# Kernel optimization log

Hardware: AMD Instinct MI355X
Metric: run time of the kernel (lower is better)

The kernel has to match this reference:

```python
import jax, jax.numpy as jnp
import numpy as np

B, N, F, W = 32, 512, 6, 128
K_GRAPH, K_POINT, HOPS = 100, 3, 2
CONV_D, POINT_D, LIN_D = 3, 3, 5
DIM2 = 2 * CONV_D * W + 2 * POINT_D * W  # 1536


def setup_inputs() -> dict:
    key = jax.random.key(0)
    ks = jax.random.split(key, 12)
    g = lambda i, shape, s=0.05: jax.random.normal(ks[i], shape, jnp.float32) * s
    return {
        'x': jax.random.normal(ks[0], (B * N, F), jnp.float32),
        'batch': jnp.repeat(jnp.arange(B, dtype=jnp.int32), N),  # equal-size graphs
        'tag1_W': g(1, (HOPS + 1, F, W)),
        'tag1_b': jnp.zeros((W,), jnp.float32),
        'tag_W': g(2, (CONV_D - 1, HOPS + 1, W, W)),
        'tag_b': jnp.zeros((CONV_D - 1, W), jnp.float32),
        'p1_W1': g(3, (2 * F, W)), 'p1_b1': jnp.zeros((W,), jnp.float32),
        'p1_W2': g(4, (W, W)), 'p1_b2': jnp.zeros((W,), jnp.float32),
        'pf_W': g(5, (POINT_D - 1, 2 * W, W)), 'pf_b': jnp.zeros((POINT_D - 1, W), jnp.float32),
        'bn_gamma': jnp.ones((DIM2,), jnp.float32), 'bn_beta': jnp.zeros((DIM2,), jnp.float32),
        'lin_W': g(6, (LIN_D, DIM2, DIM2), 0.02), 'lin_b': jnp.zeros((LIN_D, DIM2), jnp.float32),
        'out_W': g(7, (DIM2, 1)), 'out_b': jnp.zeros((1,), jnp.float32),
    }


def _knn(xb, k):
    # xb: [B,N,C] -> per-graph kNN source indices [B,N,k] (self excluded)
    sq = jnp.sum(xb * xb, axis=-1)
    d = sq[:, :, None] + sq[:, None, :] - 2.0 * jnp.einsum('bnc,bmc->bnm', xb, xb)
    d = d + jnp.eye(xb.shape[1], dtype=xb.dtype) * 1e10  # exclude self loops
    _, idx = jax.lax.top_k(-d, k)
    return idx


def _gather(xb, idx):
    # xb [B,N,C], idx [B,N,k] -> neighbor features [B,N,k,C]
    return jax.vmap(lambda xv, iv: xv[iv])(xb, idx)


def _tag(xb, nbr, Wk, b):
    # TAGConv K=2: every node has in-degree K_GRAPH, so sym gcn_norm edge weight
    # = deg^-1/2[src]*deg^-1/2[dst] = 1/k  ->  one hop == neighbor mean.
    out = jnp.einsum('bnc,cd->bnd', xb, Wk[0])
    h = xb
    for k in range(1, Wk.shape[0]):
        h = jnp.mean(_gather(h, nbr), axis=2)
        out = out + jnp.einsum('bnc,cd->bnd', h, Wk[k])
    return out + b


def _edgeconv(yb, k, mlp):
    # DynamicEdgeConv: rebuild kNN on current features, msg = mlp([x_i, x_j - x_i]), max-aggr
    nbr = _knn(yb, k)
    yj = _gather(yb, nbr)                       # [B,N,k,C]
    yi = jnp.broadcast_to(yb[:, :, None, :], yj.shape)
    m = mlp(jnp.concatenate([yi, yj - yi], axis=-1))
    return jnp.max(m, axis=2)


def reference(x, batch, tag1_W, tag1_b, tag_W, tag_b, p1_W1, p1_b1, p1_W2, p1_b2,
              pf_W, pf_b, bn_gamma, bn_beta, lin_W, lin_b, out_W, out_b):
    lrelu = jax.nn.leaky_relu  # negative_slope=0.01 matches torch default
    xb = x.reshape(B, N, -1)   # batch = repeat(arange(B), N), equal-size graphs
    nbr = _knn(xb, K_GRAPH)    # dropout_adj / Dropout: eval mode (identity)

    h = lrelu(_tag(xb, nbr, tag1_W, tag1_b))
    pools = [jnp.concatenate([h.mean(axis=1), h.max(axis=1)], axis=-1)]  # gap||gmp
    for f in range(CONV_D - 1):
        h = lrelu(_tag(h, nbr, tag_W[f], tag_b[f]))
        pools.append(jnp.concatenate([h.mean(axis=1), h.max(axis=1)], axis=-1))
    xc = jnp.concatenate(pools, axis=-1)  # [B, 2*CONV_D*W]

    mlp1 = lambda z: lrelu(lrelu(z @ p1_W1 + p1_b1) @ p1_W2 + p1_b2)
    y = _edgeconv(xb, K_POINT, mlp1)
    ylist = [y]
    for f in range(POINT_D - 1):
        y = _edgeconv(y, K_POINT, lambda z, f=f: lrelu(z @ pf_W[f] + pf_b[f]))
        ylist.append(y)
    y = jnp.concatenate(ylist, axis=-1)  # [B,N,POINT_D*W]
    yc = jnp.concatenate([y.mean(axis=1), y.max(axis=1)], axis=-1)

    z = jnp.concatenate([xc, yc], axis=-1)  # [B, DIM2]
    mu = z.mean(axis=0)
    var = jnp.mean((z - mu) ** 2, axis=0)
    z = (z - mu) / jnp.sqrt(var + 1e-5) * bn_gamma + bn_beta  # BatchNorm1d (batch stats)
    for g in range(LIN_D):
        z = lrelu(z @ lin_W[g] + lin_b[g])
    z = z @ out_W + out_b  # classification=False -> no sigmoid
    return z.reshape(-1)
```

## Files before the change

kernel.cpp:

```cpp
#include <hip/hip_runtime.h>
#include <hip/hip_bf16.h>

#define Bg 32
#define Nn 512
#define Fdim 6
#define Wd 128
#define KG 100
#define KP 3
#define DIM2 1536
#define GC16 16
#define NSL 12
#define KSL 128

typedef __hip_bfloat16 bf16;
typedef unsigned long long ull;

__device__ __forceinline__ float b2f(bf16 v) { return __bfloat162float(v); }
__device__ __forceinline__ float h2f(unsigned short h) { return __uint_as_float((unsigned)h << 16); }
__device__ __forceinline__ float lrelu(float v) { return v > 0.0f ? v : 0.01f * v; }

__global__ void detect_kernel(const unsigned short* __restrict__ x, int* __restrict__ flag) {
  if (threadIdx.x == 0 && blockIdx.x == 0) {
    int big = 0;
    for (int i = 0; i < 512; i += 2) {
      unsigned short u = x[i];
      int e = (u >> 7) & 0xFF;
      if (e >= 140) big++;
    }
    *flag = (big > 20) ? 1 : 0;
  }
}

__global__ void convert_kernel(const void* __restrict__ x, float* __restrict__ xf, int n,
                               const int* __restrict__ flag) {
  int i = blockIdx.x * 256 + threadIdx.x;
  if (i >= n) return;
  if (*flag) xf[i] = ((const float*)x)[i];
  else       xf[i] = b2f(((const bf16*)x)[i]);
}

__device__ __forceinline__ void ins3b(ull key, ull& k0, ull& k1, ull& k2) {
  ull M0 = k0 < key ? key : k0;  k0 = k0 < key ? k0 : key;
  ull M1 = k1 < M0 ? M0 : k1;    k1 = k1 < M0 ? k1 : M0;
  k2 = k2 < M1 ? k2 : M1;
}

__global__ void knn100_kernel(const float* __restrict__ xf, int* __restrict__ nbr) {
  __shared__ float xg[Nn * 7];
  __shared__ float sqv[Nn];
  int t = threadIdx.x; int w = t >> 6; int l = t & 63;
  int row0 = blockIdx.x * 4; int g = row0 >> 9;
  const float* xp = xf + g * (Nn * Fdim);
  for (int j = t; j < Nn; j += 256) {
    float s = 0.0f;
    #pragma unroll
    for (int c = 0; c < Fdim; c++) { float v = xp[j * Fdim + c]; xg[j * 7 + c] = v; s += v * v; }
    sqv[j] = s;
  }
  __syncthreads();
  int i = (row0 & 511) + w;
  float xi[Fdim];
  #pragma unroll
  for (int c = 0; c < Fdim; c++) xi[c] = xg[i * 7 + c];
  float sqi = sqv[i];
  unsigned m[8];
  #pragma unroll
  for (int ch = 0; ch < 8; ch++) {
    int j = ch * 64 + l;
    float dot = 0.0f;
    #pragma unroll
    for (int c = 0; c < Fdim; c++) dot += xi[c] * xg[j * 7 + c];
    float d = sqi + sqv[j] - 2.0f * dot;
    if (j == i) d += 1e10f;
    unsigned u = __float_as_uint(d);
    m[ch] = (u & 0x80000000u) ? ~u : (u | 0x80000000u);
  }
  unsigned T = 0u;
  for (int b = 31; b >= 0; b--) {
    unsigned mid = T | (1u << b);
    int c = 0;
    #pragma unroll
    for (int ch = 0; ch < 8; ch++) c += __popcll(__ballot(m[ch] < mid));
    if (c < KG) T = mid;
  }
  int* outp = nbr + ((size_t)(g * Nn + i)) * KG;
  ull lmask = (1ull << l) - 1ull;
  int base = 0;
  #pragma unroll
  for (int ch = 0; ch < 8; ch++) {
    bool less = m[ch] < T;
    ull bal = __ballot(less);
    if (less) outp[base + __popcll(bal & lmask)] = ch * 64 + l;
    base += __popcll(bal);
  }
  int need = KG - base;
  int eqb = 0;
  #pragma unroll
  for (int ch = 0; ch < 8; ch++) {
    bool eq = (m[ch] == T);
    ull bal = __ballot(eq);
    int gr = eqb + __popcll(bal & lmask);
    if (eq && gr < need) outp[base + gr] = ch * 64 + l;
    eqb += __popcll(bal);
  }
}

__global__ void knn3_x_kernel(const float* __restrict__ xf, int* __restrict__ nbr) {
  __shared__ float xg[Nn * 7];
  __shared__ float sqv[Nn];
  int t = threadIdx.x; int bid = blockIdx.x;
  int g = bid >> 5;
  const float* xp = xf + g * (Nn * Fdim);
  for (int j = t; j < Nn; j += 256) {
    float s = 0.0f;
    #pragma unroll
    for (int c = 0; c < Fdim; c++) { float v = xp[j * Fdim + c]; xg[j * 7 + c] = v; s += v * v; }
    sqv[j] = s;
  }
  __syncthreads();
  int lr = t >> 4; int sub = t & 15; int l = t & 63;
  int i = ((bid & 31) << 4) + lr;
  float xi[Fdim];
  #pragma unroll
  for (int c = 0; c < Fdim; c++) xi[c] = xg[i * 7 + c];
  float sqi = sqv[i];
  ull k0 = ~0ull, k1 = ~0ull, k2 = ~0ull;
  for (int jj = 0; jj < 32; jj++) {
    int s = (jj + l) & 31;
    int j = sub * 32 + s;
    float dot = 0.0f;
    #pragma unroll
    for (int c = 0; c < Fdim; c++) dot += xi[c] * xg[j * 7 + c];
    float d = sqi + sqv[j] - 2.0f * dot;
    if (j == i) d += 1e10f;
    unsigned u = __float_as_uint(d);
    unsigned m = (u & 0x80000000u) ? ~u : (u | 0x80000000u);
    ins3b(((ull)m << 32) | (unsigned)j, k0, k1, k2);
  }
  #pragma unroll
  for (int off = 1; off <= 8; off <<= 1) {
    ull b0 = __shfl_xor(k0, off, 64);
    ull b1 = __shfl_xor(k1, off, 64);
    ull b2 = __shfl_xor(k2, off, 64);
    ins3b(b0, k0, k1, k2); ins3b(b1, k0, k1, k2); ins3b(b2, k0, k1, k2);
  }
  if (sub == 0) {
    int row = g * Nn + i;
    nbr[row * 3 + 0] = (int)(k0 & 0xFFFFFFFFu);
    nbr[row * 3 + 1] = (int)(k1 & 0xFFFFFFFFu);
    nbr[row * 3 + 2] = (int)(k2 & 0xFFFFFFFFu);
  }
}

__global__ void knn3_gram_kernel(const float* __restrict__ G, int* __restrict__ nbr, int g0) {
  __shared__ float sqv[Nn];
  int t = threadIdx.x; int bid = blockIdx.x;
  int gl = bid >> 5; int g = g0 + gl;
  const float* Gg = G + (size_t)gl * Nn * Nn;
  for (int j = t; j < Nn; j += 256) sqv[j] = Gg[(size_t)j * Nn + j];
  __syncthreads();
  int lr = t >> 4; int sub = t & 15; int l = t & 63;
  int i = ((bid & 31) << 4) + lr;
  float sqi = sqv[i];
  const float* Gr = Gg + (size_t)i * Nn;
  ull k0 = ~0ull, k1 = ~0ull, k2 = ~0ull;
  for (int jj = 0; jj < 32; jj++) {
    int s = (jj + l) & 31;
    int j = sub * 32 + s;
    float d = sqi + sqv[j] - 2.0f * Gr[j];
    if (j == i) d += 1e10f;
    unsigned u = __float_as_uint(d);
    unsigned m = (u & 0x80000000u) ? ~u : (u | 0x80000000u);
    ins3b(((ull)m << 32) | (unsigned)j, k0, k1, k2);
  }
  #pragma unroll
  for (int off = 1; off <= 8; off <<= 1) {
    ull b0 = __shfl_xor(k0, off, 64);
    ull b1 = __shfl_xor(k1, off, 64);
    ull b2 = __shfl_xor(k2, off, 64);
    ins3b(b0, k0, k1, k2); ins3b(b1, k0, k1, k2); ins3b(b2, k0, k1, k2);
  }
  if (sub == 0) {
    int row = g * Nn + i;
    nbr[row * 3 + 0] = (int)(k0 & 0xFFFFFFFFu);
    nbr[row * 3 + 1] = (int)(k1 & 0xFFFFFFFFu);
    nbr[row * 3 + 2] = (int)(k2 & 0xFFFFFFFFu);
  }
}

__global__ void gm6_kernel(const float* __restrict__ src, const int* __restrict__ nbr,
                           float* __restrict__ dst) {
  __shared__ float s[Nn * Fdim];
  int g = blockIdx.x; int t = threadIdx.x;
  const float* sp = src + g * (Nn * Fdim);
  for (int idx = t; idx < Nn * Fdim; idx += 512) s[idx] = sp[idx];
  __syncthreads();
  float acc[Fdim] = {0, 0, 0, 0, 0, 0};
  const int* nb = nbr + ((size_t)(g * Nn + t)) * KG;
  for (int k = 0; k < KG; k++) {
    int j = nb[k];
    #pragma unroll
    for (int c = 0; c < Fdim; c++) acc[c] += s[j * Fdim + c];
  }
  float* dp = dst + (size_t)(g * Nn + t) * Fdim;
  #pragma unroll
  for (int c = 0; c < Fdim; c++) dp[c] = acc[c] / 100.0f;
}

__global__ void gm128_kernel(const float* __restrict__ src, const int* __restrict__ nbr,
                             float* __restrict__ dst) {
  __shared__ int ids[8][KG];
  int t = threadIdx.x;
  int row0 = blockIdx.x * 8; int g = row0 >> 9;
  for (int idx = t; idx < 8 * KG; idx += 256) {
    int r = idx / KG, k = idx - r * KG;
    ids[r][k] = nbr[(size_t)(row0 + r) * KG + k];
  }
  __syncthreads();
  int lane = t & 31, r = t >> 5;
  const float4* sp = (const float4*)(src + (size_t)g * Nn * Wd);
  float ax = 0.0f, ay = 0.0f, az = 0.0f, aw = 0.0f;
  #pragma unroll 5
  for (int k = 0; k < KG; k++) {
    float4 v = sp[ids[r][k] * 32 + lane];
    ax += v.x; ay += v.y; az += v.z; aw += v.w;
  }
  float4 o = make_float4(ax / 100.0f, ay / 100.0f, az / 100.0f, aw / 100.0f);
  ((float4*)(dst + (size_t)(row0 + r) * Wd))[lane] = o;
}

__global__ void proj3_kernel(const float* __restrict__ in0, const float* __restrict__ in1,
                             const float* __restrict__ in2, const void* __restrict__ Wt_,
                             const void* __restrict__ bt_, float* __restrict__ out,
                             const int* __restrict__ flag) {
  __shared__ float s0[48], s1[48], s2[48];
  int t = threadIdx.x;
  int node0 = blockIdx.x * 8;
  int f32 = *flag;
  float acc[8] = {0, 0, 0, 0, 0, 0, 0, 0};
  float bd;
  if (t < 48) {
    s0[t] = in0[(size_t)node0 * 6 + t];
    s1[t] = in1[(size_t)node0 * 6 + t];
    s2[t] = in2[(size_t)node0 * 6 + t];
  }
  __syncthreads();
  if (f32) {
    const float* W = (const float*)Wt_;
    for (int c = 0; c < 6; c++) {
      float w0 = W[c * 128 + t], w1 = W[(6 + c) * 128 + t], w2 = W[(12 + c) * 128 + t];
      #pragma unroll
      for (int n = 0; n < 8; n++)
        acc[n] += s0[n * 6 + c] * w0 + s1[n * 6 + c] * w1 + s2[n * 6 + c] * w2;
    }
    bd = ((const float*)bt_)[t];
  } else {
    const bf16* W = (const bf16*)Wt_;
    for (int c = 0; c < 6; c++) {
      float w0 = b2f(W[c * 128 + t]), w1 = b2f(W[(6 + c) * 128 + t]), w2 = b2f(W[(12 + c) * 128 + t]);
      #pragma unroll
      for (int n = 0; n < 8; n++)
        acc[n] += s0[n * 6 + c] * w0 + s1[n * 6 + c] * w1 + s2[n * 6 + c] * w2;
    }
    bd = b2f(((const bf16*)bt_)[t]);
  }
  #pragma unroll
  for (int n = 0; n < 8; n++)
    out[(size_t)(node0 + n) * 128 + t] = lrelu(acc[n] + bd);
}

__global__ void proj3_big_kernel(const float* __restrict__ in0, const float* __restrict__ in1,
                                 const float* __restrict__ in2, const void* __restrict__ Wt_,
                                 const void* __restrict__ bt_, float* __restrict__ out,
                                 long Woff, long boff, const int* __restrict__ flag) {
  __shared__ __align__(16) float sa[3][32 * 128];
  __shared__ __align__(16) float Wc[64 * 128];
  int t = threadIdx.x;
  int node0 = blockIdx.x * 32;
  int f32 = *flag;
  {
    const float4* q0 = (const float4*)(in0 + (size_t)node0 * 128);
    const float4* q1 = (const float4*)(in1 + (size_t)node0 * 128);
    const float4* q2 = (const float4*)(in2 + (size_t)node0 * 128);
    float4* s0 = (float4*)sa[0]; float4* s1 = (float4*)sa[1]; float4* s2 = (float4*)sa[2];
    #pragma unroll
    for (int it = 0; it < 4; it++) {
      s0[t + it * 256] = q0[t + it * 256];
      s1[t + it * 256] = q1[t + it * 256];
      s2[t + it * 256] = q2[t + it * 256];
    }
  }
  int tx = t & 31, ty = t >> 5;
  int col0 = tx * 4, n0 = ty * 4;
  float acc[4][4];
  #pragma unroll
  for (int n = 0; n < 4; n++)
    #pragma unroll
    for (int j = 0; j < 4; j++) acc[n][j] = 0.0f;
  for (int half = 0; half < 6; half++) {
    int a = half >> 1, h = half & 1;
    {
      float4* Wl = (float4*)Wc;
      if (f32) {
        const float4* Wg = (const float4*)((const float*)Wt_ + Woff
                                           + (size_t)a * 16384 + (size_t)h * 8192);
        #pragma unroll
        for (int i = 0; i < 8; i++) Wl[t + i * 256] = Wg[t + i * 256];
      } else {
        const ushort4* Wg = (const ushort4*)((const unsigned short*)Wt_ + Woff
                                             + (size_t)a * 16384 + (size_t)h * 8192);
        #pragma unroll
        for (int i = 0; i < 8; i++) {
          ushort4 hh = Wg[t + i * 256];
          Wl[t + i * 256] = make_float4(h2f(hh.x), h2f(hh.y), h2f(hh.z), h2f(hh.w));
        }
      }
    }
    __syncthreads();
    const float* sp = sa[a];
    int cbase = h * 64;
    #pragma unroll 4
    for (int cc0 = 0; cc0 < 64; cc0 += 4) {
      float wv[4][4];
      #pragma unroll
      for (int cc = 0; cc < 4; cc++) {
        float4 w4 = *(const float4*)&Wc[(cc0 + cc) * 128 + col0];
        wv[cc][0] = w4.x; wv[cc][1] = w4.y; wv[cc][2] = w4.z; wv[cc][3] = w4.w;
      }
      int c0 = cbase + cc0;
      #pragma unroll
      for (int n = 0; n < 4; n++) {
        float4 av = *(const float4*)&sp[(n0 + n) * 128 + c0];
        #pragma unroll
        for (int j = 0; j < 4; j++)
          acc[n][j] += av.x * wv[0][j] + av.y * wv[1][j] + av.z * wv[2][j] + av.w * wv[3][j];
      }
    }
    __syncthreads();
  }
  float bdv[4];
  if (f32) {
    const float* bt = (const float*)bt_ + boff;
    #pragma unroll
    for (int j = 0; j < 4; j++) bdv[j] = bt[col0 + j];
  } else {
    const bf16* bt = (const bf16*)bt_ + boff;
    #pragma unroll
    for (int j = 0; j < 4; j++) bdv[j] = b2f(bt[col0 + j]);
  }
  #pragma unroll
  for (int n = 0; n < 4; n++) {
    float4 ov;
    ov.x = lrelu(acc[n][0] + bdv[0]); ov.y = lrelu(acc[n][1] + bdv[1]);
    ov.z = lrelu(acc[n][2] + bdv[2]); ov.w = lrelu(acc[n][3] + bdv[3]);
    *(float4*)&out[(size_t)(node0 + n0 + n) * 128 + col0] = ov;
  }
}

__global__ void proj_dual_kernel(const float* __restrict__ in, const void* __restrict__ Wt_,
                                 float* __restrict__ u, float* __restrict__ v,
                                 const int* __restrict__ flag) {
  __shared__ float s0[48];
  int t = threadIdx.x; int node0 = blockIdx.x * 8;
  int f32 = *flag;
  float au[8] = {0, 0, 0, 0, 0, 0, 0, 0};
  float av[8] = {0, 0, 0, 0, 0, 0, 0, 0};
  if (t < 48) s0[t] = in[(size_t)node0 * 6 + t];
  __syncthreads();
  if (f32) {
    const float* W = (const float*)Wt_;
    for (int c = 0; c < 6; c++) {
      float wa = W[c * 128 + t], wb = W[(6 + c) * 128 + t];
      #pragma unroll
      for (int n = 0; n < 8; n++) { float x = s0[n * 6 + c]; au[n] += x * wa; av[n] += x * wb; }
    }
  } else {
    const bf16* W = (const bf16*)Wt_;
    for (int c = 0; c < 6; c++) {
      float wa = b2f(W[c * 128 + t]), wb = b2f(W[(6 + c) * 128 + t]);
      #pragma unroll
      for (int n = 0; n < 8; n++) { float x = s0[n * 6 + c]; au[n] += x * wa; av[n] += x * wb; }
    }
  }
  #pragma unroll
  for (int n = 0; n < 8; n++) {
    u[(size_t)(node0 + n) * 128 + t] = au[n];
    v[(size_t)(node0 + n) * 128 + t] = av[n];
  }
}

__global__ void proj_dual_big_kernel(const float* __restrict__ in, const void* __restrict__ Wt_,
                                     float* __restrict__ u, float* __restrict__ v,
                                     long Woff, const int* __restrict__ flag) {
  __shared__ __align__(16) float sa[32 * 128];
  __shared__ __align__(16) float Wc[64 * 128];
  int t = threadIdx.x;
  int node0 = blockIdx.x * 32;
  int f32 = *flag;
  {
    const float4* qp = (const float4*)(in + (size_t)node0 * 128);
    float4* s0 = (float4*)sa;
    #pragma unroll
    for (int it = 0; it < 4; it++) s0[t + it * 256] = qp[t + it * 256];
  }
  int tx = t & 31, ty = t >> 5;
  int col0 = tx * 4, n0 = ty * 4;
  float accu[4][4], accv[4][4];
  #pragma unroll
  for (int n = 0; n < 4; n++)
    #pragma unroll
    for (int j = 0; j < 4; j++) { accu[n][j] = 0.0f; accv[n][j] = 0.0f; }
  for (int q = 0; q < 4; q++) {
    {
      float4* Wl = (float4*)Wc;
      if (f32) {
        const float4* Wg = (const float4*)((const float*)Wt_ + Woff + (size_t)q * 8192);
        #pragma unroll
        for (int i = 0; i < 8; i++) Wl[t + i * 256] = Wg[t + i * 256];
      } else {
        const ushort4* Wg = (const ushort4*)((const unsigned short*)Wt_ + Woff
                                             + (size_t)q * 8192);
        #pragma unroll
        for (int i = 0; i < 8; i++) {
          ushort4 hh = Wg[t + i * 256];
          Wl[t + i * 256] = make_float4(h2f(hh.x), h2f(hh.y), h2f(hh.z), h2f(hh.w));
        }
      }
    }
    __syncthreads();
    int cbase = (q & 1) * 64;
    if (q < 2) {
      #pragma unroll 4
      for (int cc0 = 0; cc0 < 64; cc0 += 4) {
        float wv[4][4];
        #pragma unroll
        for (int cc = 0; cc < 4; cc++) {
          float4 w4 = *(const float4*)&Wc[(cc0 + cc) * 128 + col0];
          wv[cc][0] = w4.x; wv[cc][1] = w4.y; wv[cc][2] = w4.z; wv[cc][3] = w4.w;
        }
        int c0 = cbase + cc0;
        #pragma unroll
        for (int n = 0; n < 4; n++) {
          float4 av = *(const float4*)&sa[(n0 + n) * 128 + c0];
          #pragma unroll
          for (int j = 0; j < 4; j++)
            accu[n][j] += av.x * wv[0][j] + av.y * wv[1][j] + av.z * wv[2][j] + av.w * wv[3][j];
        }
      }
    } else {
      #pragma unroll 4
      for (int cc0 = 0; cc0 < 64; cc0 += 4) {
        float wv[4][4];
        #pragma unroll
        for (int cc = 0; cc < 4; cc++) {
          float4 w4 = *(const float4*)&Wc[(cc0 + cc) * 128 + col0];
          wv[cc][0] = w4.x; wv[cc][1] = w4.y; wv[cc][2] = w4.z; wv[cc][3] = w4.w;
        }
        int c0 = cbase + cc0;
        #pragma unroll
        for (int n = 0; n < 4; n++) {
          float4 av = *(const float4*)&sa[(n0 + n) * 128 + c0];
          #pragma unroll
          for (int j = 0; j < 4; j++)
            accv[n][j] += av.x * wv[0][j] + av.y * wv[1][j] + av.z * wv[2][j] + av.w * wv[3][j];
        }
      }
    }
    __syncthreads();
  }
  #pragma unroll
  for (int n = 0; n < 4; n++) {
    *(float4*)&u[(size_t)(node0 + n0 + n) * 128 + col0] = *(float4*)accu[n];
    *(float4*)&v[(size_t)(node0 + n0 + n) * 128 + col0] = *(float4*)accv[n];
  }
}

__global__ void edge_mlp1_kernel(const float* __restrict__ u, const float* __restrict__ v,
                                 const int* __restrict__ nbrp, const void* __restrict__ W2_,
                                 const void* __restrict__ b1_, const void* __restrict__ b2_,
                                 float* __restrict__ y, const int* __restrict__ flag) {
  __shared__ __align__(16) float Ws[64 * 128];
  __shared__ __align__(16) float tl[24][128];
  int t = threadIdx.x;
  int node0 = blockIdx.x * 8; int g = node0 >> 9;
  int f32 = *flag;
  if (f32) {
    const float4* Wg = (const float4*)W2_;
    float4* Wl = (float4*)Ws;
    #pragma unroll
    for (int i = 0; i < 8; i++) Wl[t + i * 256] = Wg[t + i * 256];
  } else {
    const ushort4* Wg = (const ushort4*)W2_;
    float4* Wl = (float4*)Ws;
    #pragma unroll
    for (int i = 0; i < 8; i++) {
      ushort4 h = Wg[t + i * 256];
      Wl[t + i * 256] = make_float4(h2f(h.x), h2f(h.y), h2f(h.z), h2f(h.w));
    }
  }
  {
    int lane = t & 31, n = t >> 5;
    int row = node0 + n;
    float4 ui = ((const float4*)(u + (size_t)row * 128))[lane];
    float4 vi = ((const float4*)(v + (size_t)row * 128))[lane];
    float4 b1v;
    if (f32) b1v = ((const float4*)b1_)[lane];
    else {
      ushort4 h = ((const ushort4*)b1_)[lane];
      b1v = make_float4(h2f(h.x), h2f(h.y), h2f(h.z), h2f(h.w));
    }
    float4 base = make_float4(ui.x - vi.x + b1v.x, ui.y - vi.y + b1v.y,
                              ui.z - vi.z + b1v.z, ui.w - vi.w + b1v.w);
    #pragma unroll
    for (int k = 0; k < 3; k++) {
      int j = nbrp[row * 3 + k];
      float4 vj = ((const float4*)(v + (size_t)(g * Nn + j) * 128))[lane];
      float4 tv;
      tv.x = lrelu(base.x + vj.x); tv.y = lrelu(base.y + vj.y);
      tv.z = lrelu(base.z + vj.z); tv.w = lrelu(base.w + vj.w);
      *(float4*)&tl[n * 3 + k][lane * 4] = tv;
    }
  }
  __syncthreads();
  int tx = t & 31, ty = t >> 5;
  int col0 = tx * 4;
  float acc[3][4];
  #pragma unroll
  for (int k = 0; k < 3; k++)
    #pragma unroll
    for (int j = 0; j < 4; j++) acc[k][j] = 0.0f;
  #pragma unroll 4
  for (int cc0 = 0; cc0 < 64; cc0 += 4) {
    float wv[4][4];
    #pragma unroll
    for (int cc = 0; cc < 4; cc++) {
      float4 w4 = *(const float4*)&Ws[(cc0 + cc) * 128 + col0];
      wv[cc][0] = w4.x; wv[cc][1] = w4.y; wv[cc][2] = w4.z; wv[cc][3] = w4.w;
    }
    #pragma unroll
    for (int k = 0; k < 3; k++) {
      float4 av = *(const float4*)&tl[ty * 3 + k][cc0];
      #pragma unroll
      for (int j = 0; j < 4; j++)
        acc[k][j] += av.x * wv[0][j] + av.y * wv[1][j] + av.z * wv[2][j] + av.w * wv[3][j];
    }
  }
  __syncthreads();
  if (f32) {
    const float4* Wg = (const float4*)W2_ + 2048;
    float4* Wl = (float4*)Ws;
    #pragma unroll
    for (int i = 0; i < 8; i++) Wl[t + i * 256] = Wg[t + i * 256];
  } else {
    const ushort4* Wg = (const ushort4*)W2_ + 2048;
    float4* Wl = (float4*)Ws;
    #pragma unroll
    for (int i = 0; i < 8; i++) {
      ushort4 h = Wg[t + i * 256];
      Wl[t + i * 256] = make_float4(h2f(h.x), h2f(h.y), h2f(h.z), h2f(h.w));
    }
  }
  __syncthreads();
  #pragma unroll 4
  for (int cc0 = 0; cc0 < 64; cc0 += 4) {
    float wv[4][4];
    #pragma unroll
    for (int cc = 0; cc < 4; cc++) {
      float4 w4 = *(const float4*)&Ws[(cc0 + cc) * 128 + col0];
      wv[cc][0] = w4.x; wv[cc][1] = w4.y; wv[cc][2] = w4.z; wv[cc][3] = w4.w;
    }
    #pragma unroll
    for (int k = 0; k < 3; k++) {
      float4 av = *(const float4*)&tl[ty * 3 + k][64 + cc0];
      #pragma unroll
      for (int j = 0; j < 4; j++)
        acc[k][j] += av.x * wv[0][j] + av.y * wv[1][j] + av.z * wv[2][j] + av.w * wv[3][j];
    }
  }
  float b2d[4];
  if (f32) {
    const float* b2p = (const float*)b2_;
    #pragma unroll
    for (int j = 0; j < 4; j++) b2d[j] = b2p[col0 + j];
  } else {
    const bf16* b2p = (const bf16*)b2_;
    #pragma unroll
    for (int j = 0; j < 4; j++) b2d[j] = b2f(b2p[col0 + j]);
  }
  float4 ov;
  {
    float m0 = lrelu(acc[0][0] + b2d[0]);
    m0 = fmaxf(m0, lrelu(acc[1][0] + b2d[0]));
    ov.x = fmaxf(m0, lrelu(acc[2][0] + b2d[0]));
    float m1 = lrelu(acc[0][1] + b2d[1]);
    m1 = fmaxf(m1, lrelu(acc[1][1] + b2d[1]));
    ov.y = fmaxf(m1, lrelu(acc[2][1] + b2d[1]));
    float m2 = lrelu(acc[0][2] + b2d[2]);
    m2 = fmaxf(m2, lrelu(acc[1][2] + b2d[2]));
    ov.z = fmaxf(m2, lrelu(acc[2][2] + b2d[2]));
    float m3 = lrelu(acc[0][3] + b2d[3]);
    m3 = fmaxf(m3, lrelu(acc[1][3] + b2d[3]));
    ov.w = fmaxf(m3, lrelu(acc[2][3] + b2d[3]));
  }
  *(float4*)&y[(size_t)(node0 + ty) * 128 + col0] = ov;
}

__global__ void edge_max_kernel(const float* __restrict__ u, const float* __restrict__ v,
                                const int* __restrict__ nbrp, const void* __restrict__ bias_,
                                float* __restrict__ y, long boff, const int* __restrict__ flag) {
  int row = blockIdx.x; int g = row >> 9; int t = threadIdx.x;
  float ui = u[(size_t)row * 128 + t], vi = v[(size_t)row * 128 + t];
  float bd;
  if (*flag) bd = ((const float*)bias_ + boff)[t]; else bd = b2f(((const bf16*)bias_ + boff)[t]);
  float m = -3.4e38f;
  #pragma unroll
  for (int k = 0; k < 3; k++) {
    int j = nbrp[row * 3 + k];
    m = fmaxf(m, lrelu(ui - vi + v[(size_t)(g * Nn + j) * 128 + t] + bd));
  }
  y[(size_t)row * 128 + t] = m;
}

__global__ void gram_kernel(const float* __restrict__ y, float* __restrict__ G, int g0) {
  __shared__ float As[64][17], Bs[64][17];
  int bid = blockIdx.x;
  int gl = bid >> 6; int tt = bid & 63; int ti = tt >> 3; int tj = tt & 7;
  int g = g0 + gl;
  int t = threadIdx.x; int tx = t & 15, ty = t >> 4;
  const float* Yg = y + (size_t)g * Nn * Wd;
  float* Gg = G + (size_t)gl * Nn * Nn;
  float c[4][4];
  #pragma unroll
  for (int p = 0; p < 4; p++)
    #pragma unroll
    for (int q = 0; q < 4; q++) c[p][q] = 0.0f;
  for (int k0 = 0; k0 < 128; k0 += 16) {
    for (int idx = t; idx < 1024; idx += 256) {
      int r = idx >> 4, cc = idx & 15;
      As[r][cc] = Yg[(ti * 64 + r) * 128 + k0 + cc];
      Bs[r][cc] = Yg[(tj * 64 + r) * 128 + k0 + cc];
    }
    __syncthreads();
    for (int kk = 0; kk < 16; kk++) {
      float a[4], bb[4];
      #pragma unroll
      for (int p = 0; p < 4; p++) a[p] = As[ty * 4 + p][kk];
      #pragma unroll
      for (int q = 0; q < 4; q++) bb[q] = Bs[tx * 4 + q][kk];
      #pragma unroll
      for (int p = 0; p < 4; p++)
        #pragma unroll
        for (int q = 0; q < 4; q++) c[p][q] += a[p] * bb[q];
    }
    __syncthreads();
  }
  #pragma unroll
  for (int p = 0; p < 4; p++)
    #pragma unroll
    for (int q = 0; q < 4; q++)
      Gg[(size_t)(ti * 64 + ty * 4 + p) * Nn + tj * 64 + tx * 4 + q] = c[p][q];
}

__global__ void pool1_kernel(const float* __restrict__ h, float* __restrict__ pp) {
  int b = blockIdx.x;
  int g = b >> 3, ch = b & 7;
  int t = threadIdx.x;
  const float* hg = h + (size_t)g * Nn * Wd + (size_t)ch * 64 * Wd;
  float s = 0.0f, m = -3.4e38f;
  #pragma unroll 4
  for (int n = 0; n < 64; n++) {
    float vv = hg[n * 128 + t];
    s += vv; m = fmaxf(m, vv);
  }
  pp[b * 256 + t] = s;
  pp[b * 256 + 128 + t] = m;
}

__global__ void pool2_kernel(const float* __restrict__ pp, float* __restrict__ z,
                             int meanoff, int maxoff) {
  int g = blockIdx.x; int t = threadIdx.x;
  float s = 0.0f, m = -3.4e38f;
  #pragma unroll
  for (int q = 0; q < 8; q++) {
    s += pp[(g * 8 + q) * 256 + t];
    m = fmaxf(m, pp[(g * 8 + q) * 256 + 128 + t]);
  }
  z[g * DIM2 + meanoff + t] = s / 512.0f;
  z[g * DIM2 + maxoff + t] = m;
}

__global__ void bn_kernel(float* __restrict__ z, const void* __restrict__ gamma,
                          const void* __restrict__ beta, const int* __restrict__ flag) {
  int c = blockIdx.x * 256 + threadIdx.x;
  if (c >= DIM2) return;
  float s = 0.0f;
  for (int r = 0; r < Bg; r++) s += z[r * DIM2 + c];
  float mu = s / 32.0f;
  float v = 0.0f;
  for (int r = 0; r < Bg; r++) { float d = z[r * DIM2 + c] - mu; v += d * d; }
  float var = v / 32.0f;
  float gm, bt;
  if (*flag) { gm = ((const float*)gamma)[c]; bt = ((const float*)beta)[c]; }
  else       { gm = b2f(((const bf16*)gamma)[c]); bt = b2f(((const bf16*)beta)[c]); }
  float scale = gm / sqrtf(var + 1e-5f);
  for (int r = 0; r < Bg; r++) z[r * DIM2 + c] = (z[r * DIM2 + c] - mu) * scale + bt;
}

__global__ void hl_part_kernel(const float* __restrict__ zin, const float* __restrict__ Pin,
                               const void* __restrict__ bin_, const void* __restrict__ W_,
                               float* __restrict__ Pout, long Woff, long binoff, int mode,
                               const int* __restrict__ flag) {
  __shared__ __align__(16) float zs[32][KSL];
  int t = threadIdx.x;
  int bd = blockIdx.x % 24, s = blockIdx.x / 24;
  int d0 = bd * 64, k0 = s * KSL;
  int f32 = *flag;
  if (mode == 0) {
    for (int idx = t; idx < 32 * KSL; idx += 256) {
      int r = idx >> 7, k = idx & 127;
      zs[r][k] = zin[r * DIM2 + k0 + k];
    }
  } else {
    for (int idx = t; idx < 32 * KSL / 4; idx += 256) {
      int r = idx >> 5, k4 = (idx & 31) * 4;
      float ax = 0.0f, ay = 0.0f, az = 0.0f, aw = 0.0f;
      const float* Pr = Pin + (size_t)r * NSL * DIM2 + k0 + k4;
      #pragma unroll
      for (int ss = 0; ss < NSL; ss++) {
        float4 p = *(const float4*)(Pr + (size_t)ss * DIM2);
        ax += p.x; ay += p.y; az += p.z; aw += p.w;
      }
      float b0, b1, b2, b3;
      if (f32) {
        const float* bp = (const float*)bin_ + binoff + k0 + k4;
        b0 = bp[0]; b1 = bp[1]; b2 = bp[2]; b3 = bp[3];
      } else {
        const bf16* bp = (const bf16*)bin_ + binoff + k0 + k4;
        b0 = b2f(bp[0]); b1 = b2f(bp[1]); b2 = b2f(bp[2]); b3 = b2f(bp[3]);
      }
      zs[r][k4 + 0] = lrelu(ax + b0);
      zs[r][k4 + 1] = lrelu(ay + b1);
      zs[r][k4 + 2] = lrelu(az + b2);
      zs[r][k4 + 3] = lrelu(aw + b3);
    }
  }
  __syncthreads();
  int lane = t & 63, rg = t >> 6;
  int d = d0 + lane, r0 = rg * 8;
  float acc[8];
  #pragma unroll
  for (int i = 0; i < 8; i++) acc[i] = 0.0f;
  if (f32) {
    const float* W = (const float*)W_ + Woff;
    for (int k = 0; k < KSL; k += 4) {
      float w0 = W[(size_t)(k0 + k) * DIM2 + d];
      float w1 = W[(size_t)(k0 + k + 1) * DIM2 + d];
      float w2 = W[(size_t)(k0 + k + 2) * DIM2 + d];
      float w3 = W[(size_t)(k0 + k + 3) * DIM2 + d];
      #pragma unroll
      for (int i = 0; i < 8; i++) {
        float4 z4 = *(const float4*)&zs[r0 + i][k];
        acc[i] += z4.x * w0 + z4.y * w1 + z4.z * w2 + z4.w * w3;
      }
    }
  } else {
    const unsigned short* W = (const unsigned short*)W_ + Woff;
    for (int k = 0; k < KSL; k += 4) {
      float w0 = h2f(W[(size_t)(k0 + k) * DIM2 + d]);
      float w1 = h2f(W[(size_t)(k0 + k + 1) * DIM2 + d]);
      float w2 = h2f(W[(size_t)(k0 + k + 2) * DIM2 + d]);
      float w3 = h2f(W[(size_t)(k0 + k + 3) * DIM2 + d]);
      #pragma unroll
      for (int i = 0; i < 8; i++) {
        float4 z4 = *(const float4*)&zs[r0 + i][k];
        acc[i] += z4.x * w0 + z4.y * w1 + z4.z * w2 + z4.w * w3;
      }
    }
  }
  float* Po = Pout + (size_t)s * DIM2 + d;
  #pragma unroll
  for (int i = 0; i < 8; i++) Po[(size_t)(r0 + i) * NSL * DIM2] = acc[i];
}

__global__ void hl_reduce_kernel(const float* __restrict__ Pin, const void* __restrict__ bin_,
                                 float* __restrict__ out, long binoff,
                                 const int* __restrict__ flag) {
  int idx = blockIdx.x * 256 + threadIdx.x;
  int r = idx / DIM2, d = idx - r * DIM2;
  float acc = 0.0f;
  const float* Pr = Pin + (size_t)r * NSL * DIM2 + d;
  #pragma unroll
  for (int s = 0; s < NSL; s++) acc += Pr[(size_t)s * DIM2];
  float b;
  if (*flag) b = ((const float*)bin_ + binoff)[d];
  else       b = b2f(((const bf16*)bin_ + binoff)[d]);
  out[r * DIM2 + d] = lrelu(acc + b);
}

__global__ void final_kernel(const float* __restrict__ zin, const void* __restrict__ outW,
                             const void* __restrict__ outb, void* __restrict__ out,
                             const int* __restrict__ flag) {
  __shared__ float red[256];
  int r = blockIdx.x, t = threadIdx.x;
  int f32 = *flag;
  float acc = 0.0f;
  if (f32) {
    const float* W = (const float*)outW;
    for (int c = t; c < DIM2; c += 256) acc += zin[r * DIM2 + c] * W[c];
  } else {
    const bf16* W = (const bf16*)outW;
    for (int c = t; c < DIM2; c += 256) acc += zin[r * DIM2 + c] * b2f(W[c]);
  }
  red[t] = acc; __syncthreads();
  for (int s = 128; s > 0; s >>= 1) { if (t < s) red[t] += red[t + s]; __syncthreads(); }
  if (t == 0) {
    float ob;
    if (f32) ob = ((const float*)outb)[0]; else ob = b2f(((const bf16*)outb)[0]);
    float val = red[0] + ob;
    if (f32) ((float*)out)[r] = val;
    else     ((bf16*)out)[r] = __float2bfloat16(val);
  }
}

extern "C" void kernel_launch(void* const* d_in, const int* in_sizes, int n_in,
                              void* d_out, int out_size, void* d_ws, size_t ws_size,
                              hipStream_t stream) {
  const void* x      = d_in[0];
  const void* tag1_W = d_in[2];
  const void* tag1_b = d_in[3];
  const void* tag_W  = d_in[4];
  const void* tag_b  = d_in[5];
  const void* p1_W1  = d_in[6];
  const void* p1_b1  = d_in[7];
  const void* p1_W2  = d_in[8];
  const void* p1_b2  = d_in[9];
  const void* pf_W   = d_in[10];
  const void* pf_b   = d_in[11];
  const void* bn_g   = d_in[12];
  const void* bn_b   = d_in[13];
  const void* lin_W  = d_in[14];
  const void* lin_b  = d_in[15];
  const void* out_W  = d_in[16];
  const void* out_b  = d_in[17];

  float* ws = (float*)d_ws;
  float* XF   = ws + 0;
  float* M16  = ws + 98304;
  float* M26  = ws + 196608;
  float* Z    = ws + 294912;
  float* ZB   = ws + 344064;
  int*   FLAG = (int*)(ws + 409600);
  int*   NBRP = (int*)(ws + 409616);
  int*   NBRG = (int*)(ws + 458768);
  float* S0   = ws + 2097168;
  float* S1   = ws + 4194320;
  float* S2   = ws + 6291472;
  float* S3   = ws + 8388624;
  float* PA   = S0;
  float* PB   = S1;
  float* PP   = M16;

  detect_kernel<<<1, 64, 0, stream>>>((const unsigned short*)x, FLAG);
  convert_kernel<<<384, 256, 0, stream>>>(x, XF, Bg * Nn * Fdim, FLAG);
  knn100_kernel<<<Bg * Nn / 4, 256, 0, stream>>>(XF, NBRG);
  knn3_x_kernel<<<Bg * Nn / 16, 256, 0, stream>>>(XF, NBRP);

  gm6_kernel<<<Bg, 512, 0, stream>>>(XF, NBRG, M16);
  gm6_kernel<<<Bg, 512, 0, stream>>>(M16, NBRG, M26);
  proj3_kernel<<<2048, 128, 0, stream>>>(XF, M16, M26, tag1_W, tag1_b, S0, FLAG);
  pool1_kernel<<<256, 128, 0, stream>>>(S0, PP);
  pool2_kernel<<<Bg, 128, 0, stream>>>(PP, Z, 0, 128);

  gm128_kernel<<<Bg * Nn / 8, 256, 0, stream>>>(S0, NBRG, S1);
  gm128_kernel<<<Bg * Nn / 8, 256, 0, stream>>>(S1, NBRG, S2);
  proj3_big_kernel<<<512, 256, 0, stream>>>(S0, S1, S2, tag_W, tag_b, S3, 0, 0, FLAG);
  pool1_kernel<<<256, 128, 0, stream>>>(S3, PP);
  pool2_kernel<<<Bg, 128, 0, stream>>>(PP, Z, 256, 384);

  gm128_kernel<<<Bg * Nn / 8, 256, 0, stream>>>(S3, NBRG, S1);
  gm128_kernel<<<Bg * Nn / 8, 256, 0, stream>>>(S1, NBRG, S2);
  proj3_big_kernel<<<512, 256, 0, stream>>>(S3, S1, S2, tag_W, tag_b, S0,
                                            3L * 128 * 128, 128, FLAG);
  pool1_kernel<<<256, 128, 0, stream>>>(S0, PP);
  pool2_kernel<<<Bg, 128, 0, stream>>>(PP, Z, 512, 640);

  proj_dual_kernel<<<2048, 128, 0, stream>>>(XF, p1_W1, S0, S1, FLAG);
  edge_mlp1_kernel<<<2048, 256, 0, stream>>>(S0, S1, NBRP, p1_W2, p1_b1, p1_b2, S2, FLAG);
  pool1_kernel<<<256, 128, 0, stream>>>(S2, PP);
  pool2_kernel<<<Bg, 128, 0, stream>>>(PP, Z, 768, 1152);

  for (int c = 0; c < Bg; c += GC16) {
    gram_kernel<<<GC16 * 64, 256, 0, stream>>>(S2, S0, c);
    knn3_gram_kernel<<<GC16 * Nn / 16, 256, 0, stream>>>(S0, NBRP, c);
  }
  proj_dual_big_kernel<<<512, 256, 0, stream>>>(S2, pf_W, S0, S1, 0, FLAG);
  edge_max_kernel<<<Bg * Nn, 128, 0, stream>>>(S0, S1, NBRP, pf_b, S3, 0, FLAG);
  pool1_kernel<<<256, 128, 0, stream>>>(S3, PP);
  pool2_kernel<<<Bg, 128, 0, stream>>>(PP, Z, 896, 1280);

  for (int c = 0; c < Bg; c += GC16) {
    gram_kernel<<<GC16 * 64, 256, 0, stream>>>(S3, S0, c);
    knn3_gram_kernel<<<GC16 * Nn / 16, 256, 0, stream>>>(S0, NBRP, c);
  }
  proj_dual_big_kernel<<<512, 256, 0, stream>>>(S3, pf_W, S0, S1, 256L * 128, FLAG);
  edge_max_kernel<<<Bg * Nn, 128, 0, stream>>>(S0, S1, NBRP, pf_b, S2, 128, FLAG);
  pool1_kernel<<<256, 128, 0, stream>>>(S2, PP);
  pool2_kernel<<<Bg, 128, 0, stream>>>(PP, Z, 1024, 1408);

  bn_kernel<<<6, 256, 0, stream>>>(Z, bn_g, bn_b, FLAG);
  hl_part_kernel<<<288, 256, 0, stream>>>(Z, nullptr, nullptr, lin_W, PA,
                                          0L * DIM2 * DIM2, 0L, 0, FLAG);
  hl_part_kernel<<<288, 256, 0, stream>>>(nullptr, PA, lin_b, lin_W, PB,
                                          1L * DIM2 * DIM2, 0L * DIM2, 1, FLAG);
  hl_part_kernel<<<288, 256, 0, stream>>>(nullptr, PB, lin_b, lin_W, PA,
                                          2L * DIM2 * DIM2, 1L * DIM2, 1, FLAG);
  hl_part_kernel<<<288, 256, 0, stream>>>(nullptr, PA, lin_b, lin_W, PB,
                                          3L * DIM2 * DIM2, 2L * DIM2, 1, FLAG);
  hl_part_kernel<<<288, 256, 0, stream>>>(nullptr, PB, lin_b, lin_W, PA,
                                          4L * DIM2 * DIM2, 3L * DIM2, 1, FLAG);
  hl_reduce_kernel<<<192, 256, 0, stream>>>(PA, lin_b, ZB, 4L * DIM2, FLAG);
  final_kernel<<<Bg, 256, 0, stream>>>(ZB, out_W, out_b, d_out, FLAG);
}
```

Baseline: 842.5 us.

## Enlarge edge_mlp1 tile to 32 nodes with 6x8 register blocking

```diff
diff --git a/kernel.cpp b/kernel.cpp
--- a/kernel.cpp
+++ b/kernel.cpp
@@ -480,9 +480,9 @@
                                  const void* __restrict__ b1_, const void* __restrict__ b2_,
                                  float* __restrict__ y, const int* __restrict__ flag) {
   __shared__ __align__(16) float Ws[64 * 128];
-  __shared__ __align__(16) float tl[24][128];
+  __shared__ __align__(16) float tl[96][128];
   int t = threadIdx.x;
-  int node0 = blockIdx.x * 8; int g = node0 >> 9;
+  int node0 = blockIdx.x * 32; int g = node0 >> 9;
   int f32 = *flag;
   if (f32) {
     const float4* Wg = (const float4*)W2_;
@@ -499,50 +499,56 @@
     }
   }
   {
-    int lane = t & 31, n = t >> 5;
-    int row = node0 + n;
-    float4 ui = ((const float4*)(u + (size_t)row * 128))[lane];
-    float4 vi = ((const float4*)(v + (size_t)row * 128))[lane];
+    int lane = t & 31, grp = t >> 5;
     float4 b1v;
     if (f32) b1v = ((const float4*)b1_)[lane];
     else {
       ushort4 h = ((const ushort4*)b1_)[lane];
       b1v = make_float4(h2f(h.x), h2f(h.y), h2f(h.z), h2f(h.w));
     }
-    float4 base = make_float4(ui.x - vi.x + b1v.x, ui.y - vi.y + b1v.y,
-                              ui.z - vi.z + b1v.z, ui.w - vi.w + b1v.w);
-    #pragma unroll
-    for (int k = 0; k < 3; k++) {
-      int j = nbrp[row * 3 + k];
-      float4 vj = ((const float4*)(v + (size_t)(g * Nn + j) * 128))[lane];
-      float4 tv;
-      tv.x = lrelu(base.x + vj.x); tv.y = lrelu(base.y + vj.y);
-      tv.z = lrelu(base.z + vj.z); tv.w = lrelu(base.w + vj.w);
-      *(float4*)&tl[n * 3 + k][lane * 4] = tv;
-    }
-  }
-  __syncthreads();
-  int tx = t & 31, ty = t >> 5;
-  int col0 = tx * 4;
-  float acc[3][4];
-  #pragma unroll
-  for (int k = 0; k < 3; k++)
-    #pragma unroll
-    for (int j = 0; j < 4; j++) acc[k][j] = 0.0f;
-  #pragma unroll 4
+    #pragma unroll
+    for (int nn = 0; nn < 4; nn++) {
+      int n = grp * 4 + nn;
+      int row = node0 + n;
+      float4 ui = ((const float4*)(u + (size_t)row * 128))[lane];
+      float4 vi = ((const float4*)(v + (size_t)row * 128))[lane];
+      float4 base = make_float4(ui.x - vi.x + b1v.x, ui.y - vi.y + b1v.y,
+                                ui.z - vi.z + b1v.z, ui.w - vi.w + b1v.w);
+      #pragma unroll
+      for (int k = 0; k < 3; k++) {
+        int j = nbrp[row * 3 + k];
+        float4 vj = ((const float4*)(v + (size_t)(g * Nn + j) * 128))[lane];
+        float4 tv;
+        tv.x = lrelu(base.x + vj.x); tv.y = lrelu(base.y + vj.y);
+        tv.z = lrelu(base.z + vj.z); tv.w = lrelu(base.w + vj.w);
+        *(float4*)&tl[n * 3 + k][lane * 4] = tv;
+      }
+    }
+  }
+  __syncthreads();
+  int tx = t & 15, ty = t >> 4;
+  int col0 = tx * 8;
+  int r0 = ty * 6;
+  float acc[6][8];
+  #pragma unroll
+  for (int r = 0; r < 6; r++)
+    #pragma unroll
+    for (int j = 0; j < 8; j++) acc[r][j] = 0.0f;
   for (int cc0 = 0; cc0 < 64; cc0 += 4) {
-    float wv[4][4];
+    float wv[4][8];
     #pragma unroll
     for (int cc = 0; cc < 4; cc++) {
-      float4 w4 = *(const float4*)&Ws[(cc0 + cc) * 128 + col0];
-      wv[cc][0] = w4.x; wv[cc][1] = w4.y; wv[cc][2] = w4.z; wv[cc][3] = w4.w;
-    }
-    #pragma unroll
-    for (int k = 0; k < 3; k++) {
-      float4 av = *(const float4*)&tl[ty * 3 + k][cc0];
-      #pragma unroll
-      for (int j = 0; j < 4; j++)
-        acc[k][j] += av.x * wv[0][j] + av.y * wv[1][j] + av.z * wv[2][j] + av.w * wv[3][j];
+      float4 wa = *(const float4*)&Ws[(cc0 + cc) * 128 + col0];
+      float4 wb = *(const float4*)&Ws[(cc0 + cc) * 128 + col0 + 4];
+      wv[cc][0] = wa.x; wv[cc][1] = wa.y; wv[cc][2] = wa.z; wv[cc][3] = wa.w;
+      wv[cc][4] = wb.x; wv[cc][5] = wb.y; wv[cc][6] = wb.z; wv[cc][7] = wb.w;
+    }
+    #pragma unroll
+    for (int r = 0; r < 6; r++) {
+      float4 av = *(const float4*)&tl[r0 + r][cc0];
+      #pragma unroll
+      for (int j = 0; j < 8; j++)
+        acc[r][j] += av.x * wv[0][j] + av.y * wv[1][j] + av.z * wv[2][j] + av.w * wv[3][j];
     }
   }
   __syncthreads();
@@ -561,48 +567,47 @@
     }
   }
   __syncthreads();
-  #pragma unroll 4
   for (int cc0 = 0; cc0 < 64; cc0 += 4) {
-    float wv[4][4];
+    float wv[4][8];
     #pragma unroll
     for (int cc = 0; cc < 4; cc++) {
-      float4 w4 = *(const float4*)&Ws[(cc0 + cc) * 128 + col0];
-      wv[cc][0] = w4.x; wv[cc][1] = w4.y; wv[cc][2] = w4.z; wv[cc][3] = w4.w;
-    }
-    #pragma unroll
-    for (int k = 0; k < 3; k++) {
-      float4 av = *(const float4*)&tl[ty * 3 + k][64 + cc0];
-      #pragma unroll
-      for (int j = 0; j < 4; j++)
-        acc[k][j] += av.x * wv[0][j] + av.y * wv[1][j] + av.z * wv[2][j] + av.w * wv[3][j];
-    }
-  }
-  float b2d[4];
+      float4 wa = *(const float4*)&Ws[(cc0 + cc) * 128 + col0];
+      float4 wb = *(const float4*)&Ws[(cc0 + cc) * 128 + col0 + 4];
+      wv[cc][0] = wa.x; wv[cc][1] = wa.y; wv[cc][2] = wa.z; wv[cc][3] = wa.w;
+      wv[cc][4] = wb.x; wv[cc][5] = wb.y; wv[cc][6] = wb.z; wv[cc][7] = wb.w;
+    }
+    #pragma unroll
+    for (int r = 0; r < 6; r++) {
+      float4 av = *(const float4*)&tl[r0 + r][64 + cc0];
+      #pragma unroll
+      for (int j = 0; j < 8; j++)
+        acc[r][j] += av.x * wv[0][j] + av.y * wv[1][j] + av.z * wv[2][j] + av.w * wv[3][j];
+    }
+  }
+  float b2d[8];
   if (f32) {
     const float* b2p = (const float*)b2_;
     #pragma unroll
-    for (int j = 0; j < 4; j++) b2d[j] = b2p[col0 + j];
+    for (int j = 0; j < 8; j++) b2d[j] = b2p[col0 + j];
   } else {
     const bf16* b2p = (const bf16*)b2_;
     #pragma unroll
-    for (int j = 0; j < 4; j++) b2d[j] = b2f(b2p[col0 + j]);
-  }
-  float4 ov;
-  {
-    float m0 = lrelu(acc[0][0] + b2d[0]);
-    m0 = fmaxf(m0, lrelu(acc[1][0] + b2d[0]));
-    ov.x = fmaxf(m0, lrelu(acc[2][0] + b2d[0]));
-    float m1 = lrelu(acc[0][1] + b2d[1]);
-    m1 = fmaxf(m1, lrelu(acc[1][1] + b2d[1]));
-    ov.y = fmaxf(m1, lrelu(acc[2][1] + b2d[1]));
-    float m2 = lrelu(acc[0][2] + b2d[2]);
-    m2 = fmaxf(m2, lrelu(acc[1][2] + b2d[2]));
-    ov.z = fmaxf(m2, lrelu(acc[2][2] + b2d[2]));
-    float m3 = lrelu(acc[0][3] + b2d[3]);
-    m3 = fmaxf(m3, lrelu(acc[1][3] + b2d[3]));
-    ov.w = fmaxf(m3, lrelu(acc[2][3] + b2d[3]));
-  }
-  *(float4*)&y[(size_t)(node0 + ty) * 128 + col0] = ov;
+    for (int j = 0; j < 8; j++) b2d[j] = b2f(b2p[col0 + j]);
+  }
+  #pragma unroll
+  for (int a = 0; a < 2; a++) {
+    int rb = a * 3;
+    float o[8];
+    #pragma unroll
+    for (int j = 0; j < 8; j++) {
+      float m = lrelu(acc[rb][j] + b2d[j]);
+      m = fmaxf(m, lrelu(acc[rb + 1][j] + b2d[j]));
+      o[j] = fmaxf(m, lrelu(acc[rb + 2][j] + b2d[j]));
+    }
+    float* yp = &y[(size_t)(node0 + 2 * ty + a) * 128 + col0];
+    *(float4*)yp = make_float4(o[0], o[1], o[2], o[3]);
+    *(float4*)(yp + 4) = make_float4(o[4], o[5], o[6], o[7]);
+  }
 }
 
 __global__ void edge_max_kernel(const float* __restrict__ u, const float* __restrict__ v,
@@ -885,7 +890,7 @@
   pool2_kernel<<<Bg, 128, 0, stream>>>(PP, Z, 512, 640);
 
   proj_dual_kernel<<<2048, 128, 0, stream>>>(XF, p1_W1, S0, S1, FLAG);
-  edge_mlp1_kernel<<<2048, 256, 0, stream>>>(S0, S1, NBRP, p1_W2, p1_b1, p1_b2, S2, FLAG);
+  edge_mlp1_kernel<<<512, 256, 0, stream>>>(S0, S1, NBRP, p1_W2, p1_b1, p1_b2, S2, FLAG);
   pool1_kernel<<<256, 128, 0, stream>>>(S2, PP);
   pool2_kernel<<<Bg, 128, 0, stream>>>(PP, Z, 768, 1152);
 
```

After: 855.9 us. Within noise of the previous version (+1.6%).
